# Kernel tuning notes

Measured on AMD Instinct MI355X. Metric: run time of the kernel, lower is better.

## Reference

```python
import jax, jax.numpy as jnp
import numpy as np

C1, C2 = 32, 16  # first_no_layer, second_no_layer
BN_EPS = 1e-5


def _irr(x, W, b):
    # Faithful port of irregular_convolution.forward.
    # x: [B, S, C, N, K] (torch layout with an extra seq axis).
    # torch: permute(0,1,3,2) then reshape([B, N, C*K]) -- a logical row-major
    # reshape of the transposed tensor (identical semantics in jnp).
    B, S, C, N, K = x.shape
    t = jnp.swapaxes(x, -1, -2).reshape(B, S, N, C * K)
    y = jnp.einsum('bsnm,om->bsno', t, W) + b  # tiny GEMM
    # permute(0,2,1).unsqueeze(-1) -> [B, S, O, N, 1]
    return jnp.moveaxis(y, -1, 2)[..., None]


def _prepare(y, neigh):
    # Faithful port of prepare_data: broadcast node row then masked_select.
    # y: [B, S, C, 1, N]; masked_select with a row-sorted kernel mask is a gather
    # of each node's sorted semantic neighbors: out[...,n,k] = y[...,0,neigh[n,k]].
    v = y[..., 0, :]          # [B, S, C, N]
    return v[..., neigh]      # [B, S, C, N, K]


def setup_inputs() -> dict:
    key = jax.random.key(0)
    ks = jax.random.split(key, 10)
    B, S, N, K = 8, 24, 4096, 9
    inp = {
        'input': jax.random.normal(ks[0], (B, S, N, K), dtype=jnp.float32),
        'neigh': jnp.sort(jax.random.randint(ks[1], (N, K), 0, N), axis=-1).astype(jnp.int32),
        'W1': jax.random.normal(ks[2], (C1, 1 * K), dtype=jnp.float32) * 0.05,
        'b1': jax.random.normal(ks[3], (C1,), dtype=jnp.float32) * 0.05,
        'W2': jax.random.normal(ks[4], (C2, C1 * K), dtype=jnp.float32) * 0.05,
        'b2': jax.random.normal(ks[5], (C2,), dtype=jnp.float32) * 0.05,
        'gamma': jnp.ones((C2,), dtype=jnp.float32),
        'beta': jnp.zeros((C2,), dtype=jnp.float32),
        'W3': jax.random.normal(ks[6], (1, C2 * K), dtype=jnp.float32) * 0.05,
        'b3': jax.random.normal(ks[7], (1,), dtype=jnp.float32) * 0.05,
    }
    return inp


def reference(input, neigh, W1, b1, W2, b2, gamma, beta, W3, b3):
    x = input[:, :, None]                                   # [B,S,1,N,K]
    h = jax.nn.relu(_irr(x, W1, b1))                        # [B,S,32,N,1]
    h = jnp.swapaxes(h, -1, -2)                             # [B,S,32,1,N]
    g = _prepare(h, neigh)                                  # [B,S,32,N,K]
    y = _irr(g, W2, b2)                                     # [B,S,16,N,1]
    # BatchNorm2d (training mode): stats over batch+spatial, per seq step & channel
    mean = jnp.mean(y, axis=(0, 3, 4), keepdims=True)
    var = jnp.var(y, axis=(0, 3, 4), keepdims=True)
    gb = (1, 1, C2, 1, 1)
    y = gamma.reshape(gb) * (y - mean) * jax.lax.rsqrt(var + BN_EPS) + beta.reshape(gb)
    y = jax.nn.relu(y)
    y = jnp.swapaxes(y, -1, -2)                             # [B,S,16,1,N]
    g = _prepare(y, neigh)                                  # [B,S,16,N,K]
    y = jax.nn.relu(_irr(g, W3, b3))                        # [B,S,1,N,1]
    return jnp.squeeze(y, axis=(2, 4))                      # [B,S,N]
```

## Files before the change

kernel.cpp:

```cpp
#include <hip/hip_runtime.h>
#include <hip/hip_bf16.h>

#define NB 8
#define NS 24
#define NN 4096
#define NC1 32
#define NC2 16
#define BN_COUNT 32768.0f

typedef float f32x4 __attribute__((ext_vector_type(4)));
typedef short bf16x8 __attribute__((ext_vector_type(8)));
union U8 { int4 i; bf16x8 b; };
union Q  { uint4 v; unsigned u[4]; };

#define PERM_LO 0x05040100u
#define PERM_HI 0x07060302u

__device__ __forceinline__ unsigned short bfbits(float x) {
    __hip_bfloat16 h = __float2bfloat16(x);
    return *(unsigned short*)&h;
}

__global__ __launch_bounds__(256) void k_prep(const float* __restrict__ input,
                                              float* __restrict__ flatT,
                                              const int* __restrict__ neigh,
                                              int* __restrict__ G2M,
                                              int* __restrict__ G3M,
                                              const float* __restrict__ W2,
                                              const float* __restrict__ W3,
                                              __hip_bfloat16* __restrict__ W2B,
                                              __hip_bfloat16* __restrict__ W3B) {
    __shared__ __align__(16) float tile[9216];
    int blk = blockIdx.x;
    if (blk >= 768) {
        int j = (blk - 768) * 256 + threadIdx.x;
        if (j < 36864) {
            int j8 = j & 7;
            int tkbl = j >> 3;
            int l = tkbl & 63;
            int tkb = tkbl >> 6;
            int t = tkb / 9, kb = tkb - t * 9;
            int r = t * 16 + (l & 15);
            int k = kb * 32 + ((l >> 4) << 3) + j8;
            int rem = r * 288 + k;
            G2M[j] = neigh[(rem & 4095) * 9 + (rem >> 12)];
        } else if (j < 77824) {
            int t2 = j - 36864;
            int j8 = t2 & 7;
            int tkbl = t2 >> 3;
            int l = tkbl & 63;
            int tkb = tkbl >> 6;
            int t = tkb / 5, kb = tkb - t * 5;
            int r = t * 16 + (l & 15);
            int k = kb * 32 + ((l >> 4) << 3) + j8;
            int rem = r * 144 + k;
            G3M[t2] = (k < 144) ? neigh[(rem & 4095) * 9 + (rem >> 12)] : 0;
        } else if (j < 82432) {
            int jj = j - 77824;
            int kb = jj >> 9;
            int rest = jj & 511;
            int l = rest >> 3, j8 = rest & 7;
            int o = l & 15;
            int k = kb * 32 + ((l >> 4) << 3) + j8;
            W2B[jj] = __float2bfloat16(W2[o * 288 + k]);
        } else {
            int jj = j - 82432;
            int kb = jj >> 9;
            int rest = jj & 511;
            int l = rest >> 3, j8 = rest & 7;
            int o = l & 15;
            int k = kb * 32 + ((l >> 4) << 3) + j8;
            W3B[jj] = __float2bfloat16((o == 0 && k < 144) ? W3[k] : 0.f);
        }
        return;
    }

    int bs = blk >> 2, tt = blk & 3;
    int n0 = tt << 10;
    const float4* src = (const float4*)(input + (size_t)bs * 36864 + (size_t)n0 * 9);
    float4* tp = (float4*)tile;
    for (int j = threadIdx.x; j < 2304; j += 256) tp[j] = src[j];
    __syncthreads();
    float* dst = flatT + (size_t)bs * 36864 + n0;
    for (int j = threadIdx.x; j < 2304; j += 256) {
        int k = j >> 8, u = j & 255;
        float4 w;
        w.x = tile[(u * 4 + 0) * 9 + k];
        w.y = tile[(u * 4 + 1) * 9 + k];
        w.z = tile[(u * 4 + 2) * 9 + k];
        w.w = tile[(u * 4 + 3) * 9 + k];
        *(float4*)(dst + k * 4096 + u * 4) = w;
    }
}

__global__ __launch_bounds__(512, 4) void k_l12(const float* __restrict__ flatT,
                                                const float* __restrict__ W1,
                                                const float* __restrict__ b1,
                                                const int4* __restrict__ G2M4,
                                                const int4* __restrict__ W2B4,
                                                const float* __restrict__ b2,
                                                __hip_bfloat16* __restrict__ y2p,
                                                float* __restrict__ psum,
                                                float* __restrict__ psq) {
    __shared__ __align__(16) uint4 hl[4096];
    __shared__ float wred[2][8][16];
    int blk = blockIdx.x;
    int pl = blk / 192;
    int bs = blk - pl * 192;

    int tid = threadIdx.x;
    int l = tid & 63, w = tid >> 6;
    int o = l & 15, q = l >> 4;

    const int4* gp = G2M4 + (size_t)(w * 9) * 128 + l * 2;
    int4 ia = gp[0];
    int4 ib = gp[1];
    U8 bf; bf.i = W2B4[l];

    const float* T = flatT + (size_t)bs * 36864;
    const float* W1s = W1 + pl * 72;
    float b1v[8];
#pragma unroll
    for (int c = 0; c < 8; c++) b1v[c] = b1[pl * 8 + c];

#pragma unroll 2
    for (int j = 0; j < 8; j++) {
        int p = tid + 512 * j;
        const float* tp = T + p * 9;
        float v[9];
#pragma unroll
        for (int m = 0; m < 9; m++) v[m] = tp[m];
        uint4 d;
        unsigned* dp = (unsigned*)&d;
#pragma unroll
        for (int pr = 0; pr < 4; pr++) {
            float a0 = b1v[2 * pr], a1 = b1v[2 * pr + 1];
#pragma unroll
            for (int m = 0; m < 9; m++) a0 = fmaf(v[m], W1s[(2 * pr) * 9 + m], a0);
#pragma unroll
            for (int m = 0; m < 9; m++) a1 = fmaf(v[m], W1s[(2 * pr + 1) * 9 + m], a1);
            dp[pr] = (unsigned)bfbits(fmaxf(a0, 0.f)) |
                     ((unsigned)bfbits(fmaxf(a1, 0.f)) << 16);
        }
        hl[p] = d;
    }
    __syncthreads();

    float bb = b2[o];
    float s1 = 0.f, s2 = 0.f;
    __hip_bfloat16* ypl = y2p + (((size_t)(o >> 3) * 192 + bs) * NN) * 8 + (o & 7);

    f32x4 acc[8];
#pragma unroll
    for (int c = 0; c < 8; c++) acc[c] = (f32x4){0.f, 0.f, 0.f, 0.f};

#pragma unroll
    for (int kb = 0; kb < 9; kb++) {
        int4 na, nb; U8 nbf;
        if (kb < 8) {
            na = gp[(kb + 1) * 128];
            nb = gp[(kb + 1) * 128 + 1];
            nbf.i = W2B4[(kb + 1) * 64 + l];
        }
        Q d[8];
        d[0].v = hl[ia.x]; d[1].v = hl[ia.y]; d[2].v = hl[ia.z]; d[3].v = hl[ia.w];
        d[4].v = hl[ib.x]; d[5].v = hl[ib.y]; d[6].v = hl[ib.z]; d[7].v = hl[ib.w];
#pragma unroll
        for (int c = 0; c < 8; c++) {
            const int q2 = c >> 1;
            const unsigned sel = (c & 1) ? PERM_HI : PERM_LO;
            U8 Af;
            Af.i.x = __builtin_amdgcn_perm(d[1].u[q2], d[0].u[q2], sel);
            Af.i.y = __builtin_amdgcn_perm(d[3].u[q2], d[2].u[q2], sel);
            Af.i.z = __builtin_amdgcn_perm(d[5].u[q2], d[4].u[q2], sel);
            Af.i.w = __builtin_amdgcn_perm(d[7].u[q2], d[6].u[q2], sel);
            acc[c] = __builtin_amdgcn_mfma_f32_16x16x32_bf16(Af.b, bf.b, acc[c], 0, 0, 0);
        }
        if (kb < 8) { ia = na; ib = nb; bf = nbf; }
    }

    int rbase = w * 16 + q * 4;
#pragma unroll
    for (int c = 0; c < 8; c++) {
        int C = pl * 8 + c;
#pragma unroll
        for (int i = 0; i < 4; i++) {
            float v = acc[c][i] + bb;
            s1 += v; s2 += v * v;
            int n = C * 128 + rbase + i;
            ypl[(size_t)n * 8] = __float2bfloat16(v);
        }
    }

    s1 += __shfl_xor(s1, 16); s1 += __shfl_xor(s1, 32);
    s2 += __shfl_xor(s2, 16); s2 += __shfl_xor(s2, 32);
    if (l < 16) { wred[0][w][l] = s1; wred[1][w][l] = s2; }
    __syncthreads();
    if (tid < 16) {
        float a = 0.f, b = 0.f;
#pragma unroll
        for (int ww = 0; ww < 8; ww++) { a += wred[0][ww][tid]; b += wred[1][ww][tid]; }
        int srow = (bs % NS) * 16 + tid;
        int col  = (bs / NS) * 4 + pl;
        psum[srow * 32 + col] = a;
        psq [srow * 32 + col] = b;
    }
}

__global__ __launch_bounds__(512, 4) void k_l3bn(const uint4* __restrict__ y2p,
                                                 const int4* __restrict__ G3M4,
                                                 const int4* __restrict__ W3B4,
                                                 const float* __restrict__ psum,
                                                 const float* __restrict__ psq,
                                                 const float* __restrict__ gamma,
                                                 const float* __restrict__ beta,
                                                 const float* __restrict__ b3,
                                                 float* __restrict__ out) {
    __shared__ __align__(16) uint4 zl[4096];
    __shared__ float scl[8], shf[8];
    int blk = blockIdx.x;
    int oct = blk & 1, bs = blk >> 1;
    int s = bs % NS;
    int tid = threadIdx.x;

    if (tid < 256) {
        int jj = tid >> 5, col = tid & 31;
        int row = s * 16 + oct * 8 + jj;
        float sv = psum[row * 32 + col];
        float qv = psq [row * 32 + col];
        for (int off = 16; off; off >>= 1) {
            sv += __shfl_down(sv, off, 32);
            qv += __shfl_down(qv, off, 32);
        }
        if (col == 0) {
            float mean = sv * (1.0f / BN_COUNT);
            float var  = qv * (1.0f / BN_COUNT) - mean * mean;
            float inv  = rsqrtf(var + 1e-5f);
            int o = oct * 8 + jj;
            float scv = gamma[o] * inv;
            scl[jj] = scv;
            shf[jj] = beta[o] - mean * scv;
        }
    }
    __syncthreads();

    float sc[8], sh[8];
#pragma unroll
    for (int jj = 0; jj < 8; jj++) { sc[jj] = scl[jj]; sh[jj] = shf[jj]; }

    int l = tid & 63, w = tid >> 6;
    int o = l & 15, q = l >> 4;

    const int4* gp0 = G3M4 + (size_t)(w * 5) * 128 + l * 2;
    int4 ia = gp0[0];
    int4 ib = gp0[1];
    U8 bf; bf.i = W3B4[l];

    const uint4* yb = y2p + ((size_t)oct * 192 + bs) * NN;
    for (int j = tid; j < 4096; j += 512) {
        uint4 u = yb[j];
        unsigned r[4] = {u.x, u.y, u.z, u.w};
        uint4 pk;
        unsigned* pp = (unsigned*)&pk;
#pragma unroll
        for (int dd = 0; dd < 4; dd++) {
            float lo = fmaxf(fmaf(__uint_as_float(r[dd] << 16),         sc[dd*2],   sh[dd*2]),   0.f);
            float hi = fmaxf(fmaf(__uint_as_float(r[dd] & 0xffff0000u), sc[dd*2+1], sh[dd*2+1]), 0.f);
            unsigned ulo = __float_as_uint(lo) + 0x8000u;
            unsigned uhi = __float_as_uint(hi) + 0x8000u;
            pp[dd] = __builtin_amdgcn_perm(uhi, ulo, PERM_HI);
        }
        zl[j] = pk;
    }
    __syncthreads();

    float b3v = b3[0];

#pragma unroll
    for (int tt = 0; tt < 2; tt++) {
        int t = tt * 8 + w;
        const int4* gp = G3M4 + (size_t)(t * 5) * 128 + l * 2;
        f32x4 acc[8];
#pragma unroll
        for (int c = 0; c < 8; c++) acc[c] = (f32x4){0.f, 0.f, 0.f, 0.f};
#pragma unroll
        for (int kb = 0; kb < 5; kb++) {
            int4 na, nb; U8 nbf;
            if (kb < 4) {
                na = gp[(kb + 1) * 128];
                nb = gp[(kb + 1) * 128 + 1];
                nbf.i = W3B4[(kb + 1) * 64 + l];
            } else if (tt == 0) {
                const int4* gpn = G3M4 + (size_t)((8 + w) * 5) * 128 + l * 2;
                na = gpn[0];
                nb = gpn[1];
                nbf.i = W3B4[l];
            }
            Q d[8];
            d[0].v = zl[ia.x]; d[1].v = zl[ia.y]; d[2].v = zl[ia.z]; d[3].v = zl[ia.w];
            d[4].v = zl[ib.x]; d[5].v = zl[ib.y]; d[6].v = zl[ib.z]; d[7].v = zl[ib.w];
#pragma unroll
            for (int c = 0; c < 8; c++) {
                const int q2 = c >> 1;
                const unsigned sel = (c & 1) ? PERM_HI : PERM_LO;
                U8 Af;
                Af.i.x = __builtin_amdgcn_perm(d[1].u[q2], d[0].u[q2], sel);
                Af.i.y = __builtin_amdgcn_perm(d[3].u[q2], d[2].u[q2], sel);
                Af.i.z = __builtin_amdgcn_perm(d[5].u[q2], d[4].u[q2], sel);
                Af.i.w = __builtin_amdgcn_perm(d[7].u[q2], d[6].u[q2], sel);
                acc[c] = __builtin_amdgcn_mfma_f32_16x16x32_bf16(Af.b, bf.b, acc[c], 0, 0, 0);
            }
            if (kb < 4 || tt == 0) { ia = na; ib = nb; bf = nbf; }
        }
        if (o == 0) {
            int rbase = t * 16 + q * 4;
            float* ob = out + (size_t)bs * NN + oct * 2048;
#pragma unroll
            for (int c = 0; c < 8; c++)
#pragma unroll
                for (int i = 0; i < 4; i++)
                    ob[c * 256 + rbase + i] = fmaxf(acc[c][i] + b3v, 0.f);
        }
    }
}

extern "C" void kernel_launch(void* const* d_in, const int* in_sizes, int n_in,
                              void* d_out, int out_size, void* d_ws, size_t ws_size,
                              hipStream_t stream) {
    const float* input = (const float*)d_in[0];
    const int*   neigh = (const int*)d_in[1];
    const float* W1    = (const float*)d_in[2];
    const float* b1    = (const float*)d_in[3];
    const float* W2    = (const float*)d_in[4];
    const float* b2    = (const float*)d_in[5];
    const float* gamma = (const float*)d_in[6];
    const float* beta  = (const float*)d_in[7];
    const float* W3    = (const float*)d_in[8];
    const float* b3    = (const float*)d_in[9];
    float* out = (float*)d_out;

    char* ws = (char*)d_ws;
    int*            G2M   = (int*)            (ws);
    int*            G3M   = (int*)            (ws + 147456);
    __hip_bfloat16* W2B   = (__hip_bfloat16*) (ws + 311296);
    __hip_bfloat16* W3B   = (__hip_bfloat16*) (ws + 320512);
    float*          flatT = (float*)          (ws + 325632);
    __hip_bfloat16* y2    = (__hip_bfloat16*) (ws + 28637184);
    float*          psum  = (float*)          (ws + 53803008);
    float*          psq   = (float*)          (ws + 53852160);

    k_prep<<<1100, 256, 0, stream>>>(input, flatT, neigh, G2M, G3M,
                                     W2, W3, W2B, W3B);
    k_l12<<<768, 512, 0, stream>>>(flatT, W1, b1, (const int4*)G2M,
                                   (const int4*)W2B, b2, y2, psum, psq);
    k_l3bn<<<384, 512, 0, stream>>>((const uint4*)y2, (const int4*)G3M,
                                    (const int4*)W3B, psum, psq,
                                    gamma, beta, b3, out);
}
```

Before: 131.9 us.

## Permute LDS node layout so each thread loads contiguous input vectors

Each thread now processes 8 consecutive nodes and reads their 72 input floats as nine 16-byte vector loads instead of scalar strided loads. To keep the LDS writes coalesced, the shared-memory node index is swizzled (node p stored at (p&7)*512 + p>>3). The precomputed gather index tables are remapped through the same swizzle, and the stage-3 LDS fill applies it too. The gather address pattern in LDS changes, which may alter bank-conflict behaviour. Global reads become per-thread contiguous rather than coalesced across a wavefront.

Measured after the change: 139.7 us. 5.9% more time.

```diff
diff --git a/kernel.cpp b/kernel.cpp
--- a/kernel.cpp
+++ b/kernel.cpp
@@ -15,6 +15,8 @@
 
 #define PERM_LO 0x05040100u
 #define PERM_HI 0x07060302u
+
+#define SIG(x) ((((x) & 7) << 9) | ((x) >> 3))
 
 __device__ __forceinline__ unsigned short bfbits(float x) {
     __hip_bfloat16 h = __float2bfloat16(x);
@@ -43,7 +45,7 @@
             int r = t * 16 + (l & 15);
             int k = kb * 32 + ((l >> 4) << 3) + j8;
             int rem = r * 288 + k;
-            G2M[j] = neigh[(rem & 4095) * 9 + (rem >> 12)];
+            G2M[j] = SIG(neigh[(rem & 4095) * 9 + (rem >> 12)]);
         } else if (j < 77824) {
             int t2 = j - 36864;
             int j8 = t2 & 7;
@@ -54,7 +56,7 @@
             int r = t * 16 + (l & 15);
             int k = kb * 32 + ((l >> 4) << 3) + j8;
             int rem = r * 144 + k;
-            G3M[t2] = (k < 144) ? neigh[(rem & 4095) * 9 + (rem >> 12)] : 0;
+            G3M[t2] = (k < 144) ? SIG(neigh[(rem & 4095) * 9 + (rem >> 12)]) : 0;
         } else if (j < 82432) {
             int jj = j - 77824;
             int kb = jj >> 9;
@@ -123,26 +125,34 @@
 #pragma unroll
     for (int c = 0; c < 8; c++) b1v[c] = b1[pl * 8 + c];
 
-#pragma unroll 2
-    for (int j = 0; j < 8; j++) {
-        int p = tid + 512 * j;
-        const float* tp = T + p * 9;
-        float v[9];
-#pragma unroll
-        for (int m = 0; m < 9; m++) v[m] = tp[m];
-        uint4 d;
-        unsigned* dp = (unsigned*)&d;
-#pragma unroll
-        for (int pr = 0; pr < 4; pr++) {
-            float a0 = b1v[2 * pr], a1 = b1v[2 * pr + 1];
-#pragma unroll
-            for (int m = 0; m < 9; m++) a0 = fmaf(v[m], W1s[(2 * pr) * 9 + m], a0);
-#pragma unroll
-            for (int m = 0; m < 9; m++) a1 = fmaf(v[m], W1s[(2 * pr + 1) * 9 + m], a1);
-            dp[pr] = (unsigned)bfbits(fmaxf(a0, 0.f)) |
-                     ((unsigned)bfbits(fmaxf(a1, 0.f)) << 16);
-        }
-        hl[p] = d;
+#pragma unroll
+    for (int qd = 0; qd < 2; qd++) {
+        const f32x4* tp4 = (const f32x4*)(T + (size_t)tid * 72 + qd * 36);
+        f32x4 vv[9];
+#pragma unroll
+        for (int m = 0; m < 9; m++) vv[m] = tp4[m];
+#pragma unroll
+        for (int i = 0; i < 4; i++) {
+            uint4 d;
+            unsigned* dp = (unsigned*)&d;
+#pragma unroll
+            for (int pr = 0; pr < 4; pr++) {
+                float a0 = b1v[2 * pr], a1 = b1v[2 * pr + 1];
+#pragma unroll
+                for (int m = 0; m < 9; m++) {
+                    const int idx = i * 9 + m;
+                    a0 = fmaf(vv[idx >> 2][idx & 3], W1s[(2 * pr) * 9 + m], a0);
+                }
+#pragma unroll
+                for (int m = 0; m < 9; m++) {
+                    const int idx = i * 9 + m;
+                    a1 = fmaf(vv[idx >> 2][idx & 3], W1s[(2 * pr + 1) * 9 + m], a1);
+                }
+                dp[pr] = (unsigned)bfbits(fmaxf(a0, 0.f)) |
+                         ((unsigned)bfbits(fmaxf(a1, 0.f)) << 16);
+            }
+            hl[(qd * 4 + i) * 512 + tid] = d;
+        }
     }
     __syncthreads();
 
@@ -270,7 +280,7 @@
             unsigned uhi = __float_as_uint(hi) + 0x8000u;
             pp[dd] = __builtin_amdgcn_perm(uhi, ulo, PERM_HI);
         }
-        zl[j] = pk;
+        zl[((j & 7) << 9) | (j >> 3)] = pk;
     }
     __syncthreads();
 
```

## Drop input transpose pass; read input with remapped indexing in layer-1/2 kernel

Applied to the files above, without the earlier changes.

Removes the k_prep transpose that wrote a flatT copy of the 28 MB input. k_l12 now reads the original input directly using the (fm&4095)*9+(fm>>12) index mapping, and the table-building work becomes its own small kernel. This saves a full read plus write of the input but makes k_l12 loads strided and less coalesced. k_l3bn block ordering also changes so consecutive blocks cover different bs values rather than the two octets of the same bs.

Result: slower. 199.4 us (+51.1%).

```diff
diff --git a/kernel.cpp b/kernel.cpp
--- a/kernel.cpp
+++ b/kernel.cpp
@@ -21,79 +21,55 @@
     return *(unsigned short*)&h;
 }
 
-__global__ __launch_bounds__(256) void k_prep(const float* __restrict__ input,
-                                              float* __restrict__ flatT,
-                                              const int* __restrict__ neigh,
-                                              int* __restrict__ G2M,
-                                              int* __restrict__ G3M,
-                                              const float* __restrict__ W2,
-                                              const float* __restrict__ W3,
-                                              __hip_bfloat16* __restrict__ W2B,
-                                              __hip_bfloat16* __restrict__ W3B) {
-    __shared__ __align__(16) float tile[9216];
-    int blk = blockIdx.x;
-    if (blk >= 768) {
-        int j = (blk - 768) * 256 + threadIdx.x;
-        if (j < 36864) {
-            int j8 = j & 7;
-            int tkbl = j >> 3;
-            int l = tkbl & 63;
-            int tkb = tkbl >> 6;
-            int t = tkb / 9, kb = tkb - t * 9;
-            int r = t * 16 + (l & 15);
-            int k = kb * 32 + ((l >> 4) << 3) + j8;
-            int rem = r * 288 + k;
-            G2M[j] = neigh[(rem & 4095) * 9 + (rem >> 12)];
-        } else if (j < 77824) {
-            int t2 = j - 36864;
-            int j8 = t2 & 7;
-            int tkbl = t2 >> 3;
-            int l = tkbl & 63;
-            int tkb = tkbl >> 6;
-            int t = tkb / 5, kb = tkb - t * 5;
-            int r = t * 16 + (l & 15);
-            int k = kb * 32 + ((l >> 4) << 3) + j8;
-            int rem = r * 144 + k;
-            G3M[t2] = (k < 144) ? neigh[(rem & 4095) * 9 + (rem >> 12)] : 0;
-        } else if (j < 82432) {
-            int jj = j - 77824;
-            int kb = jj >> 9;
-            int rest = jj & 511;
-            int l = rest >> 3, j8 = rest & 7;
-            int o = l & 15;
-            int k = kb * 32 + ((l >> 4) << 3) + j8;
-            W2B[jj] = __float2bfloat16(W2[o * 288 + k]);
-        } else {
-            int jj = j - 82432;
-            int kb = jj >> 9;
-            int rest = jj & 511;
-            int l = rest >> 3, j8 = rest & 7;
-            int o = l & 15;
-            int k = kb * 32 + ((l >> 4) << 3) + j8;
-            W3B[jj] = __float2bfloat16((o == 0 && k < 144) ? W3[k] : 0.f);
-        }
-        return;
-    }
-
-    int bs = blk >> 2, tt = blk & 3;
-    int n0 = tt << 10;
-    const float4* src = (const float4*)(input + (size_t)bs * 36864 + (size_t)n0 * 9);
-    float4* tp = (float4*)tile;
-    for (int j = threadIdx.x; j < 2304; j += 256) tp[j] = src[j];
-    __syncthreads();
-    float* dst = flatT + (size_t)bs * 36864 + n0;
-    for (int j = threadIdx.x; j < 2304; j += 256) {
-        int k = j >> 8, u = j & 255;
-        float4 w;
-        w.x = tile[(u * 4 + 0) * 9 + k];
-        w.y = tile[(u * 4 + 1) * 9 + k];
-        w.z = tile[(u * 4 + 2) * 9 + k];
-        w.w = tile[(u * 4 + 3) * 9 + k];
-        *(float4*)(dst + k * 4096 + u * 4) = w;
-    }
-}
-
-__global__ __launch_bounds__(512, 4) void k_l12(const float* __restrict__ flatT,
+__global__ __launch_bounds__(256) void k_tab(const int* __restrict__ neigh,
+                                             int* __restrict__ G2M,
+                                             int* __restrict__ G3M,
+                                             const float* __restrict__ W2,
+                                             const float* __restrict__ W3,
+                                             __hip_bfloat16* __restrict__ W2B,
+                                             __hip_bfloat16* __restrict__ W3B) {
+    int j = blockIdx.x * 256 + threadIdx.x;
+    if (j < 36864) {
+        int j8 = j & 7;
+        int tkbl = j >> 3;
+        int l = tkbl & 63;
+        int tkb = tkbl >> 6;
+        int t = tkb / 9, kb = tkb - t * 9;
+        int r = t * 16 + (l & 15);
+        int k = kb * 32 + ((l >> 4) << 3) + j8;
+        int rem = r * 288 + k;
+        G2M[j] = neigh[(rem & 4095) * 9 + (rem >> 12)];
+    } else if (j < 77824) {
+        int t2 = j - 36864;
+        int j8 = t2 & 7;
+        int tkbl = t2 >> 3;
+        int l = tkbl & 63;
+        int tkb = tkbl >> 6;
+        int t = tkb / 5, kb = tkb - t * 5;
+        int r = t * 16 + (l & 15);
+        int k = kb * 32 + ((l >> 4) << 3) + j8;
+        int rem = r * 144 + k;
+        G3M[t2] = (k < 144) ? neigh[(rem & 4095) * 9 + (rem >> 12)] : 0;
+    } else if (j < 82432) {
+        int jj = j - 77824;
+        int kb = jj >> 9;
+        int rest = jj & 511;
+        int l = rest >> 3, j8 = rest & 7;
+        int o = l & 15;
+        int k = kb * 32 + ((l >> 4) << 3) + j8;
+        W2B[jj] = __float2bfloat16(W2[o * 288 + k]);
+    } else if (j < 84992) {
+        int jj = j - 82432;
+        int kb = jj >> 9;
+        int rest = jj & 511;
+        int l = rest >> 3, j8 = rest & 7;
+        int o = l & 15;
+        int k = kb * 32 + ((l >> 4) << 3) + j8;
+        W3B[jj] = __float2bfloat16((o == 0 && k < 144) ? W3[k] : 0.f);
+    }
+}
+
+__global__ __launch_bounds__(512, 4) void k_l12(const float* __restrict__ input,
                                                 const float* __restrict__ W1,
                                                 const float* __restrict__ b1,
                                                 const int4* __restrict__ G2M4,
@@ -117,7 +93,7 @@
     int4 ib = gp[1];
     U8 bf; bf.i = W2B4[l];
 
-    const float* T = flatT + (size_t)bs * 36864;
+    const float* A = input + (size_t)bs * 36864;
     const float* W1s = W1 + pl * 72;
     float b1v[8];
 #pragma unroll
@@ -126,10 +102,13 @@
 #pragma unroll 2
     for (int j = 0; j < 8; j++) {
         int p = tid + 512 * j;
-        const float* tp = T + p * 9;
+        int f = p * 9;
         float v[9];
 #pragma unroll
-        for (int m = 0; m < 9; m++) v[m] = tp[m];
+        for (int m = 0; m < 9; m++) {
+            int fm = f + m;
+            v[m] = A[(fm & 4095) * 9 + (fm >> 12)];
+        }
         uint4 d;
         unsigned* dp = (unsigned*)&d;
 #pragma unroll
@@ -219,7 +198,8 @@
     __shared__ __align__(16) uint4 zl[4096];
     __shared__ float scl[8], shf[8];
     int blk = blockIdx.x;
-    int oct = blk & 1, bs = blk >> 1;
+    int bs = blk % 192;
+    int oct = blk / 192;
     int s = bs % NS;
     int tid = threadIdx.x;
 
@@ -344,14 +324,12 @@
     int*            G3M   = (int*)            (ws + 147456);
     __hip_bfloat16* W2B   = (__hip_bfloat16*) (ws + 311296);
     __hip_bfloat16* W3B   = (__hip_bfloat16*) (ws + 320512);
-    float*          flatT = (float*)          (ws + 325632);
-    __hip_bfloat16* y2    = (__hip_bfloat16*) (ws + 28637184);
-    float*          psum  = (float*)          (ws + 53803008);
-    float*          psq   = (float*)          (ws + 53852160);
-
-    k_prep<<<1100, 256, 0, stream>>>(input, flatT, neigh, G2M, G3M,
-                                     W2, W3, W2B, W3B);
-    k_l12<<<768, 512, 0, stream>>>(flatT, W1, b1, (const int4*)G2M,
+    __hip_bfloat16* y2    = (__hip_bfloat16*) (ws + 325632);
+    float*          psum  = (float*)          (ws + 25491456);
+    float*          psq   = (float*)          (ws + 25540608);
+
+    k_tab<<<332, 256, 0, stream>>>(neigh, G2M, G3M, W2, W3, W2B, W3B);
+    k_l12<<<768, 512, 0, stream>>>(input, W1, b1, (const int4*)G2M,
                                    (const int4*)W2B, b2, y2, psum, psq);
     k_l3bn<<<384, 512, 0, stream>>>((const uint4*)y2, (const int4*)G3M,
                                     (const int4*)W3B, psum, psq,
```
